# Kernel optimization log

Measured on AMD Instinct MI355X. Metric: run time of the kernel, lower is better.

## Reference

```python
import jax, jax.numpy as jnp
import numpy as np


def setup_inputs() -> dict:
    key = jax.random.key(0)
    k1, _ = jax.random.split(key)
    N, C, T, F = 32, 128, 512, 32
    x = jax.random.normal(k1, (N, C, T, F), dtype=jnp.float32)
    sigma = jnp.ones((1,), dtype=jnp.float32)
    return {"x": x, "sigma": sigma}


def reference(x, sigma):
    # x: (N, C, T, F); pairwise squared L2 distance between the C channels
    # over the T axis, independently per (batch, filter) pair.
    N, C, T, F = x.shape
    xr = jnp.transpose(x, (0, 3, 1, 2)).reshape(N * F, C, T)  # (N*F, C, T)
    # ||a-b||^2 = ||a||^2 + ||b||^2 - 2 a.b  (GEMM-based cdist)
    sq = jnp.sum(xr * xr, axis=-1)                 # (N*F, C)
    gram = jnp.einsum('bct,bdt->bcd', xr, xr)      # (N*F, C, C)
    d2 = sq[:, :, None] + sq[:, None, :] - 2.0 * gram
    d2 = jnp.maximum(d2, 0.0)                      # guard tiny negatives
    sig = jnp.reshape(sigma, ())
    kern = jnp.exp(-d2 / (2.0 * sig * sig))        # (N*F, C, C)
    kern = kern.reshape(N, F, C, C)
    return jnp.transpose(kern, (0, 2, 3, 1))       # (N, C, C, F)
```

## Files before the change

kernel.cpp:

```cpp
#include <hip/hip_runtime.h>

typedef __attribute__((ext_vector_type(4))) float f32x4;
typedef __attribute__((ext_vector_type(8))) __bf16 bf16x8;
typedef __attribute__((address_space(1))) unsigned int gu32;
typedef __attribute__((address_space(3))) unsigned int lu32;

#define PN 32
#define PC 128
#define PT 512
#define PF 32

__device__ inline unsigned short f2bf(float x) {
  unsigned int u = __float_as_uint(x);
  return (unsigned short)((u + 0x7FFFu + ((u >> 16) & 1u)) >> 16);
}
__device__ inline float bf2f(unsigned short b) {
  return __uint_as_float(((unsigned int)b) << 16);
}

__global__ __launch_bounds__(256) void pack_kernel(const float* __restrict__ x,
                                                   unsigned short* __restrict__ xt) {
  const int nc = blockIdx.x;
  const int n = nc >> 7, c = nc & 127;
  const float4* src4 = (const float4*)(x + (size_t)nc * (PT * PF));
  __shared__ unsigned short lds[32][522];
  const int tid = threadIdx.x;

  #pragma unroll
  for (int i = 0; i < 16; ++i) {
    int idx = i * 256 + tid;
    float4 v = src4[idx];
    int flat = idx << 2;
    int t = flat >> 5, f0 = flat & 31;
    lds[f0 + 0][t] = f2bf(v.x);
    lds[f0 + 1][t] = f2bf(v.y);
    lds[f0 + 2][t] = f2bf(v.z);
    lds[f0 + 3][t] = f2bf(v.w);
  }
  __syncthreads();

  #pragma unroll
  for (int i = 0; i < 16; ++i) {
    int idx = i * 256 + tid;
    int f = idx >> 7;
    int t4 = (idx & 127) << 2;
    ushort4 v;
    v.x = lds[f][t4 + 0];
    v.y = lds[f][t4 + 1];
    v.z = lds[f][t4 + 2];
    v.w = lds[f][t4 + 3];
    ushort4* dst = (ushort4*)(xt + (((size_t)(n * PF + f) * PC + c) * PT));
    dst[idx & 127] = v;
  }
}

template <bool COAL>
__global__ __launch_bounds__(256) void gram_kernel(const unsigned short* __restrict__ xt,
                                                   const float* __restrict__ sigma,
                                                   void* __restrict__ dstv) {
  const int b = blockIdx.x;
  const int n = b >> 5, f = b & 31;
  const unsigned short* A = xt + (size_t)b * PC * PT;

  __shared__ __align__(16) unsigned short lds[2][PC * 64];
  __shared__ float sq[PC];

  const int tid = threadIdx.x;
  const int wv = tid >> 6, ln = tid & 63;
  const int r0 = (wv >> 1) * 64, c0 = (wv & 1) * 64;
  const int lr = ln & 15, lq = ln >> 4;

  f32x4 acc[4][4];
  #pragma unroll
  for (int m = 0; m < 4; ++m)
    #pragma unroll
    for (int nn = 0; nn < 4; ++nn)
      acc[m][nn] = (f32x4){0.f, 0.f, 0.f, 0.f};

  const int srow = ln >> 3;
  const int sblk = (ln & 7) ^ srow;

  #pragma unroll
  for (int i = 0; i < 4; ++i) {
    int slot = i * 4 + wv;
    int crow = slot * 8 + srow;
    const unsigned short* g = A + (size_t)crow * PT + 0 + sblk * 8;
    __builtin_amdgcn_global_load_lds((gu32*)g, (lu32*)(&lds[0][slot * 512]), 16, 0, 0);
  }
  __syncthreads();

  for (int ks = 0; ks < 8; ++ks) {
    if (ks < 7) {
      const int t1 = (ks + 1) * 64;
      #pragma unroll
      for (int i = 0; i < 4; ++i) {
        int slot = i * 4 + wv;
        int crow = slot * 8 + srow;
        const unsigned short* g = A + (size_t)crow * PT + t1 + sblk * 8;
        __builtin_amdgcn_global_load_lds((gu32*)g, (lu32*)(&lds[(ks + 1) & 1][slot * 512]), 16, 0, 0);
      }
    }
    const unsigned short* L = lds[ks & 1];
    #pragma unroll
    for (int kk = 0; kk < 64; kk += 32) {
      bf16x8 av[4], bv[4];
      #pragma unroll
      for (int m = 0; m < 4; ++m) {
        int row = r0 + m * 16 + lr;
        av[m] = *(const bf16x8*)((const char*)L + row * 128 +
                                 ((((kk >> 3) + lq) ^ (row & 7)) << 4));
      }
      #pragma unroll
      for (int m = 0; m < 4; ++m) {
        int row = c0 + m * 16 + lr;
        bv[m] = *(const bf16x8*)((const char*)L + row * 128 +
                                 ((((kk >> 3) + lq) ^ (row & 7)) << 4));
      }
      #pragma unroll
      for (int m = 0; m < 4; ++m)
        #pragma unroll
        for (int nn = 0; nn < 4; ++nn)
          acc[m][nn] = __builtin_amdgcn_mfma_f32_16x16x32_bf16(av[m], bv[nn], acc[m][nn], 0, 0, 0);
    }
    __syncthreads();
  }

  #pragma unroll
  for (int m = 0; m < 4; ++m) {
    int rowb = r0 + m * 16 + lq * 4;
    int col  = c0 + m * 16 + lr;
    #pragma unroll
    for (int j = 0; j < 4; ++j)
      if (rowb + j == col) sq[col] = acc[m][m][j];
  }
  __syncthreads();

  const float sg = sigma[0];
  const float inv = 0.5f / (sg * sg);
  #pragma unroll
  for (int m = 0; m < 4; ++m) {
    #pragma unroll
    for (int nn = 0; nn < 4; ++nn) {
      int col = c0 + nn * 16 + lr;
      #pragma unroll
      for (int j = 0; j < 4; ++j) {
        int row = r0 + m * 16 + lq * 4 + j;
        float g = acc[m][nn][j];
        float d2 = fmaxf(sq[row] + sq[col] - 2.0f * g, 0.0f);
        float v = __expf(-d2 * inv);
        if (COAL) {
          ((unsigned short*)dstv)[(size_t)b * (PC * PC) + row * PC + col] = f2bf(v);
        } else {
          ((float*)dstv)[(size_t)n * (PC * PC * PF) + ((size_t)row * PC + col) * PF + f] = v;
        }
      }
    }
  }
}

__global__ __launch_bounds__(256) void unpermute_kernel(const unsigned short* __restrict__ tmp,
                                                        float* __restrict__ out) {
  const int blk = blockIdx.x;
  const int n = blk >> 7, i = blk & 127;
  __shared__ float lds[PF][PC + 1];
  const int tid = threadIdx.x;

  const unsigned short* src = tmp + (size_t)n * PF * PC * PC + (size_t)i * PC;
  #pragma unroll
  for (int it = 0; it < 4; ++it) {
    int idx4 = it * 256 + tid;
    int fr = idx4 >> 5, j4 = (idx4 & 31) << 2;
    ushort4 v = *(const ushort4*)(src + (size_t)fr * (PC * PC) + j4);
    lds[fr][j4 + 0] = bf2f(v.x);
    lds[fr][j4 + 1] = bf2f(v.y);
    lds[fr][j4 + 2] = bf2f(v.z);
    lds[fr][j4 + 3] = bf2f(v.w);
  }
  __syncthreads();

  float4* dst4 = (float4*)(out + ((size_t)(n * PC) + i) * (PC * PF));
  #pragma unroll
  for (int it = 0; it < 4; ++it) {
    int idx4 = it * 256 + tid;
    int j = idx4 >> 3, f0 = (idx4 & 7) << 2;
    float4 v;
    v.x = lds[f0 + 0][j];
    v.y = lds[f0 + 1][j];
    v.z = lds[f0 + 2][j];
    v.w = lds[f0 + 3][j];
    dst4[idx4] = v;
  }
}

extern "C" void kernel_launch(void* const* d_in, const int* in_sizes, int n_in,
                              void* d_out, int out_size, void* d_ws, size_t ws_size,
                              hipStream_t stream) {
  const float* x = (const float*)d_in[0];
  const float* sigma = (const float*)d_in[1];
  float* out = (float*)d_out;

  unsigned short* xt = (unsigned short*)d_ws;
  const size_t xt_bytes = (size_t)PN * PF * PC * PT * 2;
  const size_t tmp_bytes = (size_t)PN * PF * PC * PC * 2;
  const bool coal = ws_size >= xt_bytes + tmp_bytes;

  hipLaunchKernelGGL(pack_kernel, dim3(PN * PC), dim3(256), 0, stream, x, xt);
  if (coal) {
    unsigned short* tmp = (unsigned short*)((char*)d_ws + xt_bytes);
    hipLaunchKernelGGL((gram_kernel<true>), dim3(PN * PF), dim3(256), 0, stream, xt, sigma, (void*)tmp);
    hipLaunchKernelGGL(unpermute_kernel, dim3(PN * PC), dim3(256), 0, stream, tmp, out);
  } else {
    hipLaunchKernelGGL((gram_kernel<false>), dim3(PN * PF), dim3(256), 0, stream, xt, sigma, (void*)out);
  }
}
```

Measured before the change: 433.4 us.

## Fuse pack, gram, and unpermute into one symmetric-tile kernel

```diff
diff --git a/kernel.cpp b/kernel.cpp
--- a/kernel.cpp
+++ b/kernel.cpp
@@ -14,8 +14,144 @@
   unsigned int u = __float_as_uint(x);
   return (unsigned short)((u + 0x7FFFu + ((u >> 16) & 1u)) >> 16);
 }
+__device__ inline unsigned pk2bf(float lo, float hi) {
+  return (unsigned)f2bf(lo) | ((unsigned)f2bf(hi) << 16);
+}
 __device__ inline float bf2f(unsigned short b) {
   return __uint_as_float(((unsigned int)b) << 16);
+}
+
+__global__ __launch_bounds__(512) void fused_kernel(const float* __restrict__ x,
+                                                    const float* __restrict__ sigma,
+                                                    float* __restrict__ out) {
+  extern __shared__ char smem[];
+
+  const int bid = blockIdx.x;
+  const int sub = bid % 12;
+  const int n   = bid / 12;
+  const int tile = sub % 3;
+  const int fg   = sub / 3;
+  const int i0 = (tile == 2) ? 64 : 0;
+  const int j0 = (tile == 0) ? 0 : 64;
+
+  const int tid = threadIdx.x;
+  const int w = tid >> 6, ln = tid & 63;
+  const int lr = ln & 15, lq = ln >> 4;
+
+  f32x4 acc[4][4];
+  f32x4 sa[4], sb[4];
+  #pragma unroll
+  for (int m = 0; m < 4; ++m) {
+    sa[m] = (f32x4){0.f, 0.f, 0.f, 0.f};
+    sb[m] = (f32x4){0.f, 0.f, 0.f, 0.f};
+    #pragma unroll
+    for (int q = 0; q < 4; ++q) acc[m][q] = (f32x4){0.f, 0.f, 0.f, 0.f};
+  }
+
+  const int fh = ln & 1;
+  const int tp = ln >> 1;
+  const size_t xbase = (size_t)n * PC * PT * PF;
+
+  for (int ks = 0; ks < 8; ++ks) {
+    const int t0 = ks * 64;
+    #pragma unroll
+    for (int it = 0; it < 16; ++it) {
+      int sr = it * 8 + w;
+      int gr = (sr < 64) ? (i0 + sr) : (j0 + sr - 64);
+      const float* rp = x + xbase + ((size_t)gr * PT + t0 + 2 * tp) * PF + fg * 8 + fh * 4;
+      float4 va = *(const float4*)rp;
+      float4 vb = *(const float4*)(rp + PF);
+      int tb = tp >> 2;
+      int ti = (tp & 3) << 1;
+      int swz = ((tb ^ (sr & 7)) << 4) + (ti << 1);
+      char* base = smem + (fh * 4) * 16384 + sr * 128 + swz;
+      *(unsigned*)(base)             = pk2bf(va.x, vb.x);
+      *(unsigned*)(base + 16384)     = pk2bf(va.y, vb.y);
+      *(unsigned*)(base + 2 * 16384) = pk2bf(va.z, vb.z);
+      *(unsigned*)(base + 3 * 16384) = pk2bf(va.w, vb.w);
+    }
+    __syncthreads();
+    const char* Lw = smem + w * 16384;
+    #pragma unroll
+    for (int kk = 0; kk < 64; kk += 32) {
+      bf16x8 av[4], bv[4];
+      #pragma unroll
+      for (int m = 0; m < 4; ++m) {
+        int ra = m * 16 + lr;
+        av[m] = *(const bf16x8*)(Lw + ra * 128 + ((((kk >> 3) + lq) ^ (ra & 7)) << 4));
+        int rb = 64 + m * 16 + lr;
+        bv[m] = *(const bf16x8*)(Lw + rb * 128 + ((((kk >> 3) + lq) ^ (rb & 7)) << 4));
+      }
+      #pragma unroll
+      for (int m = 0; m < 4; ++m) {
+        sa[m] = __builtin_amdgcn_mfma_f32_16x16x32_bf16(av[m], av[m], sa[m], 0, 0, 0);
+        sb[m] = __builtin_amdgcn_mfma_f32_16x16x32_bf16(bv[m], bv[m], sb[m], 0, 0, 0);
+        #pragma unroll
+        for (int q = 0; q < 4; ++q)
+          acc[m][q] = __builtin_amdgcn_mfma_f32_16x16x32_bf16(av[m], bv[q], acc[m][q], 0, 0, 0);
+      }
+    }
+    __syncthreads();
+  }
+
+  float* sqld = (float*)smem;
+  #pragma unroll
+  for (int m = 0; m < 4; ++m) {
+    #pragma unroll
+    for (int j = 0; j < 4; ++j) {
+      if (lq * 4 + j == lr) {
+        sqld[w * 128 + m * 16 + lr]      = sa[m][j];
+        sqld[w * 128 + 64 + m * 16 + lr] = sb[m][j];
+      }
+    }
+  }
+  __syncthreads();
+
+  const float sg = sigma[0];
+  const float inv = 0.5f / (sg * sg);
+  float* oA = (float*)(smem + 65536);
+  const size_t obase = (size_t)n * PC * PC * PF + (size_t)fg * 8;
+
+  #pragma unroll
+  for (int half = 0; half < 2; ++half) {
+    #pragma unroll
+    for (int mm = 0; mm < 2; ++mm) {
+      int m = half * 2 + mm;
+      #pragma unroll
+      for (int j = 0; j < 4; ++j) {
+        int il = m * 16 + lq * 4 + j;
+        int ilh = il & 31;
+        float si = sqld[w * 128 + il];
+        #pragma unroll
+        for (int q = 0; q < 4; ++q) {
+          int jl = q * 16 + lr;
+          float sj = sqld[w * 128 + 64 + jl];
+          float d2 = fmaxf(si + sj - 2.0f * acc[m][q][j], 0.0f);
+          oA[(ilh * 64 + jl) * 8 + w] = __expf(-d2 * inv);
+        }
+      }
+    }
+    __syncthreads();
+    for (int p = tid; p < 32 * 64; p += 512) {
+      int il = p >> 6, jl = p & 63;
+      float4 v0 = *(const float4*)(oA + (il * 64 + jl) * 8);
+      float4 v1 = *(const float4*)(oA + (il * 64 + jl) * 8 + 4);
+      size_t o = obase + ((size_t)(i0 + half * 32 + il) * PC + (j0 + jl)) * PF;
+      *(float4*)(out + o) = v0;
+      *(float4*)(out + o + 4) = v1;
+    }
+    if (tile == 1) {
+      for (int p = tid; p < 64 * 32; p += 512) {
+        int a = p >> 5, b = p & 31;
+        float4 v0 = *(const float4*)(oA + (b * 64 + a) * 8);
+        float4 v1 = *(const float4*)(oA + (b * 64 + a) * 8 + 4);
+        size_t o = obase + ((size_t)(j0 + a) * PC + (i0 + half * 32 + b)) * PF;
+        *(float4*)(out + o) = v0;
+        *(float4*)(out + o + 4) = v1;
+      }
+    }
+    __syncthreads();
+  }
 }
 
 __global__ __launch_bounds__(256) void pack_kernel(const float* __restrict__ x,
@@ -25,7 +161,6 @@
   const float4* src4 = (const float4*)(x + (size_t)nc * (PT * PF));
   __shared__ unsigned short lds[32][522];
   const int tid = threadIdx.x;
-
   #pragma unroll
   for (int i = 0; i < 16; ++i) {
     int idx = i * 256 + tid;
@@ -38,7 +173,6 @@
     lds[f0 + 3][t] = f2bf(v.w);
   }
   __syncthreads();
-
   #pragma unroll
   for (int i = 0; i < 16; ++i) {
     int idx = i * 256 + tid;
@@ -54,32 +188,26 @@
   }
 }
 
-template <bool COAL>
 __global__ __launch_bounds__(256) void gram_kernel(const unsigned short* __restrict__ xt,
                                                    const float* __restrict__ sigma,
-                                                   void* __restrict__ dstv) {
+                                                   float* __restrict__ dst) {
   const int b = blockIdx.x;
   const int n = b >> 5, f = b & 31;
   const unsigned short* A = xt + (size_t)b * PC * PT;
-
   __shared__ __align__(16) unsigned short lds[2][PC * 64];
   __shared__ float sq[PC];
-
   const int tid = threadIdx.x;
   const int wv = tid >> 6, ln = tid & 63;
   const int r0 = (wv >> 1) * 64, c0 = (wv & 1) * 64;
   const int lr = ln & 15, lq = ln >> 4;
-
   f32x4 acc[4][4];
   #pragma unroll
   for (int m = 0; m < 4; ++m)
     #pragma unroll
     for (int nn = 0; nn < 4; ++nn)
       acc[m][nn] = (f32x4){0.f, 0.f, 0.f, 0.f};
-
   const int srow = ln >> 3;
   const int sblk = (ln & 7) ^ srow;
-
   #pragma unroll
   for (int i = 0; i < 4; ++i) {
     int slot = i * 4 + wv;
@@ -88,7 +216,6 @@
     __builtin_amdgcn_global_load_lds((gu32*)g, (lu32*)(&lds[0][slot * 512]), 16, 0, 0);
   }
   __syncthreads();
-
   for (int ks = 0; ks < 8; ++ks) {
     if (ks < 7) {
       const int t1 = (ks + 1) * 64;
@@ -107,14 +234,12 @@
       #pragma unroll
       for (int m = 0; m < 4; ++m) {
         int row = r0 + m * 16 + lr;
-        av[m] = *(const bf16x8*)((const char*)L + row * 128 +
-                                 ((((kk >> 3) + lq) ^ (row & 7)) << 4));
+        av[m] = *(const bf16x8*)((const char*)L + row * 128 + ((((kk >> 3) + lq) ^ (row & 7)) << 4));
       }
       #pragma unroll
       for (int m = 0; m < 4; ++m) {
         int row = c0 + m * 16 + lr;
-        bv[m] = *(const bf16x8*)((const char*)L + row * 128 +
-                                 ((((kk >> 3) + lq) ^ (row & 7)) << 4));
+        bv[m] = *(const bf16x8*)((const char*)L + row * 128 + ((((kk >> 3) + lq) ^ (row & 7)) << 4));
       }
       #pragma unroll
       for (int m = 0; m < 4; ++m)
@@ -124,7 +249,6 @@
     }
     __syncthreads();
   }
-
   #pragma unroll
   for (int m = 0; m < 4; ++m) {
     int rowb = r0 + m * 16 + lq * 4;
@@ -134,7 +258,6 @@
       if (rowb + j == col) sq[col] = acc[m][m][j];
   }
   __syncthreads();
-
   const float sg = sigma[0];
   const float inv = 0.5f / (sg * sg);
   #pragma unroll
@@ -147,48 +270,9 @@
         int row = r0 + m * 16 + lq * 4 + j;
         float g = acc[m][nn][j];
         float d2 = fmaxf(sq[row] + sq[col] - 2.0f * g, 0.0f);
-        float v = __expf(-d2 * inv);
-        if (COAL) {
-          ((unsigned short*)dstv)[(size_t)b * (PC * PC) + row * PC + col] = f2bf(v);
-        } else {
-          ((float*)dstv)[(size_t)n * (PC * PC * PF) + ((size_t)row * PC + col) * PF + f] = v;
-        }
-      }
-    }
-  }
-}
-
-__global__ __launch_bounds__(256) void unpermute_kernel(const unsigned short* __restrict__ tmp,
-                                                        float* __restrict__ out) {
-  const int blk = blockIdx.x;
-  const int n = blk >> 7, i = blk & 127;
-  __shared__ float lds[PF][PC + 1];
-  const int tid = threadIdx.x;
-
-  const unsigned short* src = tmp + (size_t)n * PF * PC * PC + (size_t)i * PC;
-  #pragma unroll
-  for (int it = 0; it < 4; ++it) {
-    int idx4 = it * 256 + tid;
-    int fr = idx4 >> 5, j4 = (idx4 & 31) << 2;
-    ushort4 v = *(const ushort4*)(src + (size_t)fr * (PC * PC) + j4);
-    lds[fr][j4 + 0] = bf2f(v.x);
-    lds[fr][j4 + 1] = bf2f(v.y);
-    lds[fr][j4 + 2] = bf2f(v.z);
-    lds[fr][j4 + 3] = bf2f(v.w);
-  }
-  __syncthreads();
-
-  float4* dst4 = (float4*)(out + ((size_t)(n * PC) + i) * (PC * PF));
-  #pragma unroll
-  for (int it = 0; it < 4; ++it) {
-    int idx4 = it * 256 + tid;
-    int j = idx4 >> 3, f0 = (idx4 & 7) << 2;
-    float4 v;
-    v.x = lds[f0 + 0][j];
-    v.y = lds[f0 + 1][j];
-    v.z = lds[f0 + 2][j];
-    v.w = lds[f0 + 3][j];
-    dst4[idx4] = v;
+        ((float*)dst)[(size_t)n * (PC * PC * PF) + ((size_t)row * PC + col) * PF + f] = __expf(-d2 * inv);
+      }
+    }
   }
 }
 
@@ -199,17 +283,14 @@
   const float* sigma = (const float*)d_in[1];
   float* out = (float*)d_out;
 
-  unsigned short* xt = (unsigned short*)d_ws;
-  const size_t xt_bytes = (size_t)PN * PF * PC * PT * 2;
-  const size_t tmp_bytes = (size_t)PN * PF * PC * PC * 2;
-  const bool coal = ws_size >= xt_bytes + tmp_bytes;
-
-  hipLaunchKernelGGL(pack_kernel, dim3(PN * PC), dim3(256), 0, stream, x, xt);
-  if (coal) {
-    unsigned short* tmp = (unsigned short*)((char*)d_ws + xt_bytes);
-    hipLaunchKernelGGL((gram_kernel<true>), dim3(PN * PF), dim3(256), 0, stream, xt, sigma, (void*)tmp);
-    hipLaunchKernelGGL(unpermute_kernel, dim3(PN * PC), dim3(256), 0, stream, tmp, out);
+  hipError_t e = hipFuncSetAttribute((const void*)fused_kernel,
+                                     hipFuncAttributeMaxDynamicSharedMemorySize, 131072);
+  if (e == hipSuccess) {
+    hipLaunchKernelGGL(fused_kernel, dim3(PN * 12), dim3(512), 131072, stream,
+                       x, sigma, out);
   } else {
-    hipLaunchKernelGGL((gram_kernel<false>), dim3(PN * PF), dim3(256), 0, stream, xt, sigma, (void*)out);
-  }
-}
+    unsigned short* xt = (unsigned short*)d_ws;
+    hipLaunchKernelGGL(pack_kernel, dim3(PN * PC), dim3(256), 0, stream, x, xt);
+    hipLaunchKernelGGL(gram_kernel, dim3(PN * PF), dim3(256), 0, stream, xt, sigma, out);
+  }
+}
```

Result: slower. 747.3 us (+72.4%).
